# Performance work log

Measured on AMD Instinct MI355X. Metric: run time of the kernel, lower is better.

The kernel has to match this reference:

```python
import jax, jax.numpy as jnp
import numpy as np

N = 16_000_000
R_MIN = 0.0
R_MAX = 10.0
R_BINS = 50
DR = (R_MAX - R_MIN) / R_BINS


def setup_inputs() -> dict:
    key = jax.random.key(0)
    k1, k2, k3 = jax.random.split(key, 3)
    # scale positions so r_cyl (Rayleigh, scale 3) populates all bins out to r=10
    positions = jax.random.normal(k1, (N, 3), dtype=jnp.float32) * 3.0
    velocities = jax.random.normal(k2, (N, 3), dtype=jnp.float32)
    masses = jax.random.uniform(k3, (N,), dtype=jnp.float32)
    return {"positions": positions, "velocities": velocities, "masses": masses}


def reference(positions, velocities, masses):
    x, y = positions[:, 0], positions[:, 1]
    vx, vy, vz = velocities[:, 0], velocities[:, 1], velocities[:, 2]
    r_cyl = jnp.sqrt(x * x + y * y)                      # [N]
    i = jnp.floor((r_cyl - R_MIN) / DR).astype(jnp.int32)
    gd = (i >= 0) & (i < R_BINS)
    idx = jnp.where(gd, i, 0)                            # safe index for masked-out particles
    w = jnp.where(gd, masses, 0.0)                       # masked masses

    v_r = (x * vx + y * vy) / r_cyl
    v_phi = (y * vx - x * vy) / r_cyl

    # six weighted moments + mass in one fused scatter-add: feats [N, 7]
    ones = jnp.ones_like(w)
    feats = jnp.stack([ones, v_r, v_r * v_r, v_phi, v_phi * v_phi, vz, vz * vz], axis=1)
    hist = jax.ops.segment_sum(w[:, None] * feats, idx, num_segments=R_BINS)  # [R_BINS, 7]

    mass = hist[:, 0]
    m = hist[:, 1:] / mass[:, None]                      # [R_BINS, 6] means of (vr, vr2, vphi, vphi2, vz, vz2)
    vr_m, vr2, vphi_m, vphi2, vz_m, vz2 = (m[:, j] for j in range(6))
    vr_sig = jnp.sqrt(vr2 - vr_m ** 2)
    vphi_sig = jnp.sqrt(vphi2 - vphi_m ** 2)
    vz_sig = jnp.sqrt(vz2 - vz_m ** 2)

    kin = jnp.stack((vphi_m, vphi_sig, vr_m, vr_sig, vz_m, vz_sig))  # [6, R_BINS]
    return kin
```

## Files before the change

### kernel.cpp

```cpp
#include <hip/hip_runtime.h>

#define R_BINS 50
#define NFEAT 7
#define HSZ (R_BINS * NFEAT)
#define STW 264

typedef __attribute__((ext_vector_type(8))) short short8;
typedef __attribute__((ext_vector_type(4))) float f32x4;

__device__ __forceinline__ unsigned pksub(unsigned a, unsigned b) {
    unsigned d;
    asm("v_pk_sub_u16 %0, %1, %2" : "=v"(d) : "v"(a), "v"(b));
    return d;
}
__device__ __forceinline__ unsigned ohc(unsigned d, unsigned onepk) {
    unsigned m;
    asm("v_pk_min_u16 %0, %1, %2" : "=v"(m) : "v"(d), "v"(onepk));
    return m << 14;
}

struct Quad { float4 p0, p1, p2, v0, v1, v2, m; };

__global__ __launch_bounds__(256, 4) void disk_hist_kernel(
    const float* __restrict__ pos,
    const float* __restrict__ vel,
    const float* __restrict__ mass,
    float* __restrict__ ghist,
    int n)
{
    __shared__ __align__(16) unsigned short st16[2][9][STW];
    __shared__ float mg[4][HSZ];

    const int tid  = threadIdx.x;
    const int lane = tid & 63;
    const int w    = tid >> 6;
    const int col  = lane & 15;
    const int g    = lane >> 4;

    for (int i = tid; i < STW; i += 256) { st16[0][7][i] = 0; st16[1][7][i] = 0; }
    __syncthreads();

    f32x4 acc[4] = {{0,0,0,0},{0,0,0,0},{0,0,0,0},{0,0,0,0}};
    f32x4 accT   = {0,0,0,0};

    union { unsigned u[4]; short8 v; } Acst;
    Acst.u[0] = Acst.u[1] = Acst.u[2] = Acst.u[3] = 0x40004000u;

    unsigned onepk = 0x00010001u;
    asm("" : "+v"(onepk));

    const int brow = (col < NFEAT) ? col : 7;
    const int co   = (w << 6) + (g << 3);
    const unsigned short* pB0 = &st16[0][brow][co];
    const unsigned short* pB1 = &st16[1][brow][co];
    const unsigned short* pN0 = &st16[0][8][co];
    const unsigned short* pN1 = &st16[1][8][co];
    const unsigned cpk0 = (unsigned)col * 0x00010001u;
    const unsigned cpk1 = cpk0 + 0x00100010u;
    const unsigned cpk2 = cpk0 + 0x00200020u;
    const unsigned cpk3 = cpk0 + 0x00300030u;

    const int stride = gridDim.x * blockDim.x;
    const int gtid   = blockIdx.x * blockDim.x + tid;
    const int nquads = n >> 2;
    const int niter  = (nquads + stride - 1) / stride;

    const float4* pos4  = (const float4*)pos;
    const float4* vel4  = (const float4*)vel;
    const float4* mass4 = (const float4*)mass;

    #define LOADQ(DST, Q) do {                                                 \
        (DST).p0 = pos4[3*(Q)+0]; (DST).p1 = pos4[3*(Q)+1];                    \
        (DST).p2 = pos4[3*(Q)+2];                                              \
        (DST).v0 = vel4[3*(Q)+0]; (DST).v1 = vel4[3*(Q)+1];                    \
        (DST).v2 = vel4[3*(Q)+2]; (DST).m = mass4[(Q)];                        \
    } while (0)

    #define STAGE(U, X, Y, VX, VY, VZ, M, VALID) do {                          \
        float x_=(X), y_=(Y), vx_=(VX), vy_=(VY), vz_=(VZ);                    \
        float d_  = x_*x_ + y_*y_;                                             \
        float ir_ = (d_ > 0.0f) ? __builtin_amdgcn_rsqf(d_) : 0.0f;            \
        float r5_ = d_ * ir_ * 5.0f;                               \
        unsigned bu_ = (unsigned)r5_;                                          \
        float wg_ = (VALID) ? (M) : 0.0f;                                      \
        float vr_ = (x_*vx_ + y_*vy_) * ir_;                                   \
        float vp_ = (y_*vx_ - x_*vy_) * ir_;                                   \
        float f1_ = wg_*vr_, f2_ = f1_*vr_;                                    \
        float f3_ = wg_*vp_, f4_ = f3_*vp_;                                    \
        float f5_ = wg_*vz_, f6_ = f5_*vz_;                                    \
        unsigned short* sb_ = &st16[U][0][tid];                                \
        sb_[0*STW] = (unsigned short)(__builtin_bit_cast(unsigned, wg_) >> 16);\
        sb_[1*STW] = (unsigned short)(__builtin_bit_cast(unsigned, f1_) >> 16);\
        sb_[2*STW] = (unsigned short)(__builtin_bit_cast(unsigned, f2_) >> 16);\
        sb_[3*STW] = (unsigned short)(__builtin_bit_cast(unsigned, f3_) >> 16);\
        sb_[4*STW] = (unsigned short)(__builtin_bit_cast(unsigned, f4_) >> 16);\
        sb_[5*STW] = (unsigned short)(__builtin_bit_cast(unsigned, f5_) >> 16);\
        sb_[6*STW] = (unsigned short)(__builtin_bit_cast(unsigned, f6_) >> 16);\
        sb_[8*STW] = (unsigned short)bu_;                                      \
    } while (0)

    #define BATCH(Braw, Nraw) do {                                             \
        short8 Bv = __builtin_bit_cast(short8, Braw);                          \
        union { unsigned u[4]; short8 v; } A;                                  \
        A.u[0]=ohc(pksub(Nraw.x,cpk0),onepk); A.u[1]=ohc(pksub(Nraw.y,cpk0),onepk); \
        A.u[2]=ohc(pksub(Nraw.z,cpk0),onepk); A.u[3]=ohc(pksub(Nraw.w,cpk0),onepk); \
        acc[0] = __builtin_amdgcn_mfma_f32_16x16x32_bf16(A.v, Bv, acc[0],0,0,0);\
        A.u[0]=ohc(pksub(Nraw.x,cpk1),onepk); A.u[1]=ohc(pksub(Nraw.y,cpk1),onepk); \
        A.u[2]=ohc(pksub(Nraw.z,cpk1),onepk); A.u[3]=ohc(pksub(Nraw.w,cpk1),onepk); \
        acc[1] = __builtin_amdgcn_mfma_f32_16x16x32_bf16(A.v, Bv, acc[1],0,0,0);\
        A.u[0]=ohc(pksub(Nraw.x,cpk2),onepk); A.u[1]=ohc(pksub(Nraw.y,cpk2),onepk); \
        A.u[2]=ohc(pksub(Nraw.z,cpk2),onepk); A.u[3]=ohc(pksub(Nraw.w,cpk2),onepk); \
        acc[2] = __builtin_amdgcn_mfma_f32_16x16x32_bf16(A.v, Bv, acc[2],0,0,0);\
        A.u[0]=ohc(pksub(Nraw.x,cpk3),onepk); A.u[1]=ohc(pksub(Nraw.y,cpk3),onepk); \
        A.u[2]=ohc(pksub(Nraw.z,cpk3),onepk); A.u[3]=ohc(pksub(Nraw.w,cpk3),onepk); \
        acc[3] = __builtin_amdgcn_mfma_f32_16x16x32_bf16(A.v, Bv, acc[3],0,0,0);\
        accT   = __builtin_amdgcn_mfma_f32_16x16x32_bf16(Acst.v, Bv, accT,0,0,0);\
    } while (0)

    #define CONSUME0() do {                                                    \
        uint4 Br0_ = *(const uint4*)pB0;  uint4 Nr0_ = *(const uint4*)pN0;     \
        uint4 Br1_ = *(const uint4*)(pB0+32); uint4 Nr1_ = *(const uint4*)(pN0+32); \
        BATCH(Br0_, Nr0_); BATCH(Br1_, Nr1_);                                  \
    } while (0)
    #define CONSUME1() do {                                                    \
        uint4 Br0_ = *(const uint4*)pB1;  uint4 Nr0_ = *(const uint4*)pN1;     \
        uint4 Br1_ = *(const uint4*)(pB1+32); uint4 Nr1_ = *(const uint4*)(pN1+32); \
        BATCH(Br0_, Nr0_); BATCH(Br1_, Nr1_);                                  \
    } while (0)

    Quad c, nx;
    LOADQ(c, gtid);
    bool cvalid = true;
    STAGE(0, c.p0.x, c.p0.y, c.v0.x, c.v0.y, c.v0.z, c.m.x, cvalid);

    for (int it = 0; it < niter; ++it) {
        int qn_raw = (it + 1) * stride + gtid;
        bool nvalid = qn_raw < nquads;
        int qn = nvalid ? qn_raw : (nquads - 1);
        LOADQ(nx, qn);

        STAGE(1, c.p0.w, c.p1.x, c.v0.w, c.v1.x, c.v1.y, c.m.y, cvalid);
        CONSUME0();
        STAGE(0, c.p1.z, c.p1.w, c.v1.z, c.v1.w, c.v2.x, c.m.z, cvalid);
        CONSUME1();
        STAGE(1, c.p2.y, c.p2.z, c.v2.y, c.v2.z, c.v2.w, c.m.w, cvalid);
        CONSUME0();
        c = nx; cvalid = nvalid;
        STAGE(0, c.p0.x, c.p0.y, c.v0.x, c.v0.y, c.v0.z, c.m.x, cvalid);
        CONSUME1();
    }

    if (col < NFEAT) {
        #pragma unroll
        for (int t = 0; t < 4; ++t) {
            #pragma unroll
            for (int r = 0; r < 4; ++r) {
                int bin = 16*t + 4*g + r;
                if (bin < R_BINS)
                    mg[w][bin * NFEAT + col] = (accT[r] - acc[t][r]) * 0.5f;
            }
        }
    }
    __syncthreads();

    for (int i = tid; i < HSZ; i += blockDim.x) {
        float s = mg[0][i] + mg[1][i] + mg[2][i] + mg[3][i];
        atomicAdd(ghist + i, s);
    }

    if (blockIdx.x == 0 && tid < (n & 3)) {
        int p = ((n >> 2) << 2) + tid;
        float x = pos[3*p], y = pos[3*p + 1];
        float r = sqrtf(x*x + y*y);
        int bin = (int)floorf(r * 5.0f);
        if (bin >= 0 && bin < R_BINS && r > 0.0f) {
            float invr = 1.0f / r;
            float vxs = vel[3*p], vys = vel[3*p+1], vzs = vel[3*p+2];
            float vr = (x*vxs + y*vys) * invr;
            float vp = (y*vxs - x*vys) * invr;
            float wg = mass[p];
            float* bptr = ghist + bin * NFEAT;
            atomicAdd(bptr + 0, wg);
            atomicAdd(bptr + 1, wg * vr);
            atomicAdd(bptr + 2, wg * vr * vr);
            atomicAdd(bptr + 3, wg * vp);
            atomicAdd(bptr + 4, wg * vp * vp);
            atomicAdd(bptr + 5, wg * vzs);
            atomicAdd(bptr + 6, wg * vzs * vzs);
        }
    }
}

__global__ void disk_finalize_kernel(const float* __restrict__ gh,
                                     float* __restrict__ out)
{
    int b = threadIdx.x;
    if (b >= R_BINS) return;
    const float* s = gh + b * NFEAT;
    float inv  = 1.0f / s[0];
    float vr_m = s[1] * inv, vr2 = s[2] * inv;
    float vp_m = s[3] * inv, vp2 = s[4] * inv;
    float vz_m = s[5] * inv, vz2 = s[6] * inv;
    out[0 * R_BINS + b] = vp_m;
    out[1 * R_BINS + b] = sqrtf(vp2 - vp_m * vp_m);
    out[2 * R_BINS + b] = vr_m;
    out[3 * R_BINS + b] = sqrtf(vr2 - vr_m * vr_m);
    out[4 * R_BINS + b] = vz_m;
    out[5 * R_BINS + b] = sqrtf(vz2 - vz_m * vz_m);
}

extern "C" void kernel_launch(void* const* d_in, const int* in_sizes, int n_in,
                              void* d_out, int out_size, void* d_ws, size_t ws_size,
                              hipStream_t stream)
{
    const float* pos  = (const float*)d_in[0];
    const float* vel  = (const float*)d_in[1];
    const float* mass = (const float*)d_in[2];
    float* out   = (float*)d_out;
    float* ghist = (float*)d_ws;
    int n = in_sizes[2];

    hipMemsetAsync(ghist, 0, HSZ * sizeof(float), stream);

    disk_hist_kernel<<<2048, 256, 0, stream>>>(pos, vel, mass, ghist, n);
    disk_finalize_kernel<<<1, 64, 0, stream>>>(ghist, out);
}
```

Baseline: 104.9 us.

## Process two quads per loop iteration with four LDS staging buffers

Restructures the main loop so each thread handles two interleaved quads (stride apart) per iteration, doubling the LDS staging buffers from two to four. STAGE and CONSUME steps of the two quads are interleaved to give more independent work between LDS writes and MFMA reads. It is meant to add memory and ALU parallelism per wave. The next-quad loads are now issued just before their first use instead of a full iteration ahead, which can expose global load latency. The extra shared memory could also limit occupancy.

After: 129.0 us. +22.9%, slower.

```diff
diff --git a/kernel.cpp b/kernel.cpp
--- a/kernel.cpp
+++ b/kernel.cpp
@@ -28,7 +28,7 @@
     float* __restrict__ ghist,
     int n)
 {
-    __shared__ __align__(16) unsigned short st16[2][9][STW];
+    __shared__ __align__(16) unsigned short st16[4][9][STW];
     __shared__ float mg[4][HSZ];
 
     const int tid  = threadIdx.x;
@@ -37,7 +37,10 @@
     const int col  = lane & 15;
     const int g    = lane >> 4;
 
-    for (int i = tid; i < STW; i += 256) { st16[0][7][i] = 0; st16[1][7][i] = 0; }
+    for (int i = tid; i < STW; i += 256) {
+        st16[0][7][i] = 0; st16[1][7][i] = 0;
+        st16[2][7][i] = 0; st16[3][7][i] = 0;
+    }
     __syncthreads();
 
     f32x4 acc[4] = {{0,0,0,0},{0,0,0,0},{0,0,0,0},{0,0,0,0}};
@@ -53,8 +56,12 @@
     const int co   = (w << 6) + (g << 3);
     const unsigned short* pB0 = &st16[0][brow][co];
     const unsigned short* pB1 = &st16[1][brow][co];
+    const unsigned short* pB2 = &st16[2][brow][co];
+    const unsigned short* pB3 = &st16[3][brow][co];
     const unsigned short* pN0 = &st16[0][8][co];
     const unsigned short* pN1 = &st16[1][8][co];
+    const unsigned short* pN2 = &st16[2][8][co];
+    const unsigned short* pN3 = &st16[3][8][co];
     const unsigned cpk0 = (unsigned)col * 0x00010001u;
     const unsigned cpk1 = cpk0 + 0x00100010u;
     const unsigned cpk2 = cpk0 + 0x00200020u;
@@ -63,7 +70,7 @@
     const int stride = gridDim.x * blockDim.x;
     const int gtid   = blockIdx.x * blockDim.x + tid;
     const int nquads = n >> 2;
-    const int niter  = (nquads + stride - 1) / stride;
+    const int niter  = (nquads + 2*stride - 1) / (2*stride);
 
     const float4* pos4  = (const float4*)pos;
     const float4* vel4  = (const float4*)vel;
@@ -117,37 +124,45 @@
         accT   = __builtin_amdgcn_mfma_f32_16x16x32_bf16(Acst.v, Bv, accT,0,0,0);\
     } while (0)
 
-    #define CONSUME0() do {                                                    \
-        uint4 Br0_ = *(const uint4*)pB0;  uint4 Nr0_ = *(const uint4*)pN0;     \
-        uint4 Br1_ = *(const uint4*)(pB0+32); uint4 Nr1_ = *(const uint4*)(pN0+32); \
+    #define CONSUME(U) do {                                                    \
+        uint4 Br0_ = *(const uint4*)pB##U;      uint4 Nr0_ = *(const uint4*)pN##U; \
+        uint4 Br1_ = *(const uint4*)(pB##U+32); uint4 Nr1_ = *(const uint4*)(pN##U+32); \
         BATCH(Br0_, Nr0_); BATCH(Br1_, Nr1_);                                  \
     } while (0)
-    #define CONSUME1() do {                                                    \
-        uint4 Br0_ = *(const uint4*)pB1;  uint4 Nr0_ = *(const uint4*)pN1;     \
-        uint4 Br1_ = *(const uint4*)(pB1+32); uint4 Nr1_ = *(const uint4*)(pN1+32); \
-        BATCH(Br0_, Nr0_); BATCH(Br1_, Nr1_);                                  \
-    } while (0)
-
-    Quad c, nx;
-    LOADQ(c, gtid);
-    bool cvalid = true;
-    STAGE(0, c.p0.x, c.p0.y, c.v0.x, c.v0.y, c.v0.z, c.m.x, cvalid);
+
+    Quad a, b;
+    bool cvA = true;
+    bool cvB = (stride + gtid) < nquads;
+    {
+        int qb0 = cvB ? (stride + gtid) : (nquads - 1);
+        LOADQ(a, gtid);
+        LOADQ(b, qb0);
+    }
+    STAGE(0, a.p0.x, a.p0.y, a.v0.x, a.v0.y, a.v0.z, a.m.x, cvA);
+    STAGE(2, b.p0.x, b.p0.y, b.v0.x, b.v0.y, b.v0.z, b.m.x, cvB);
 
     for (int it = 0; it < niter; ++it) {
-        int qn_raw = (it + 1) * stride + gtid;
-        bool nvalid = qn_raw < nquads;
-        int qn = nvalid ? qn_raw : (nquads - 1);
-        LOADQ(nx, qn);
-
-        STAGE(1, c.p0.w, c.p1.x, c.v0.w, c.v1.x, c.v1.y, c.m.y, cvalid);
-        CONSUME0();
-        STAGE(0, c.p1.z, c.p1.w, c.v1.z, c.v1.w, c.v2.x, c.m.z, cvalid);
-        CONSUME1();
-        STAGE(1, c.p2.y, c.p2.z, c.v2.y, c.v2.z, c.v2.w, c.m.w, cvalid);
-        CONSUME0();
-        c = nx; cvalid = nvalid;
-        STAGE(0, c.p0.x, c.p0.y, c.v0.x, c.v0.y, c.v0.z, c.m.x, cvalid);
-        CONSUME1();
+        STAGE(1, a.p0.w, a.p1.x, a.v0.w, a.v1.x, a.v1.y, a.m.y, cvA);
+        STAGE(3, b.p0.w, b.p1.x, b.v0.w, b.v1.x, b.v1.y, b.m.y, cvB);
+        CONSUME(0); CONSUME(2);
+        STAGE(0, a.p1.z, a.p1.w, a.v1.z, a.v1.w, a.v2.x, a.m.z, cvA);
+        STAGE(2, b.p1.z, b.p1.w, b.v1.z, b.v1.w, b.v2.x, b.m.z, cvB);
+        CONSUME(1); CONSUME(3);
+        STAGE(1, a.p2.y, a.p2.z, a.v2.y, a.v2.z, a.v2.w, a.m.w, cvA);
+        STAGE(3, b.p2.y, b.p2.z, b.v2.y, b.v2.z, b.v2.w, b.m.w, cvB);
+        CONSUME(0); CONSUME(2);
+        {
+            int qa_raw = (it + 1) * (stride << 1) + gtid;
+            int qb_raw = qa_raw + stride;
+            bool nvA = qa_raw < nquads;
+            bool nvB = qb_raw < nquads;
+            LOADQ(a, nvA ? qa_raw : (nquads - 1));
+            LOADQ(b, nvB ? qb_raw : (nquads - 1));
+            cvA = nvA; cvB = nvB;
+        }
+        STAGE(0, a.p0.x, a.p0.y, a.v0.x, a.v0.y, a.v0.z, a.m.x, cvA);
+        STAGE(2, b.p0.x, b.p0.y, b.v0.x, b.v0.y, b.v0.z, b.m.x, cvB);
+        CONSUME(1); CONSUME(3);
     }
 
     if (col < NFEAT) {
```
